# Performance work log

Hardware: AMD Instinct MI355X
Metric: run time of the kernel (lower is better)

Reference implementation:

```python
import jax, jax.numpy as jnp
import numpy as np

DIM = 2048
N_HEADS = 16
N_KV_HEADS = 8
HEAD_DIM = DIM // N_HEADS  # 128
N_REP = N_HEADS // N_KV_HEADS
THETA = 10000.0


def _rope_cos_sin(seq_len, head_dim):
    # freqs_cis = polar(1, outer(t, 1/theta^(2i/d))), i in [0, head_dim//2)
    inv = 1.0 / (THETA ** (jnp.arange(0, head_dim, 2, dtype=jnp.float32) / head_dim))
    t = jnp.arange(seq_len, dtype=jnp.float32)
    freqs = jnp.outer(t, inv)  # [S, hd/2]
    return jnp.cos(freqs), jnp.sin(freqs)


def _apply_rope(x, cos, sin):
    # x: [B, S, H, hd]; pairs (even, odd) treated as complex and multiplied by e^{i*freq}
    xr = x[..., 0::2]
    xi = x[..., 1::2]
    c = cos[None, :, None, :]
    s = sin[None, :, None, :]
    out_r = xr * c - xi * s
    out_i = xr * s + xi * c
    return jnp.stack([out_r, out_i], axis=-1).reshape(x.shape)


def setup_inputs() -> dict:
    key = jax.random.key(0)
    ks = jax.random.split(key, 5)
    B, S = 2, 2048
    sc = 0.02
    return {
        "x": jax.random.normal(ks[0], (B, S, DIM), dtype=jnp.float32),
        "wq": jax.random.normal(ks[1], (N_HEADS * HEAD_DIM, DIM), dtype=jnp.float32) * sc,
        "wk": jax.random.normal(ks[2], (N_KV_HEADS * HEAD_DIM, DIM), dtype=jnp.float32) * sc,
        "wv": jax.random.normal(ks[3], (N_KV_HEADS * HEAD_DIM, DIM), dtype=jnp.float32) * sc,
        "wo": jax.random.normal(ks[4], (DIM, N_HEADS * HEAD_DIM), dtype=jnp.float32) * sc,
        "start_pos": 0,
        "inference": 0,
    }


def reference(x, wq, wk, wv, wo, start_pos, inference):
    B, S, _ = x.shape
    xq = (x @ wq.T).reshape(B, S, N_HEADS, HEAD_DIM)
    xk = (x @ wk.T).reshape(B, S, N_KV_HEADS, HEAD_DIM)
    xv = (x @ wv.T).reshape(B, S, N_KV_HEADS, HEAD_DIM)

    cos, sin = _rope_cos_sin(S, HEAD_DIM)
    xq = _apply_rope(xq, cos, sin)
    xk = _apply_rope(xk, cos, sin)

    # repeat_kv (GQA): [B,S,Hkv,hd] -> [B,S,Hkv*n_rep,hd]
    xk = jnp.repeat(xk, N_REP, axis=2)
    xv = jnp.repeat(xv, N_REP, axis=2)

    q = xq.transpose(0, 2, 1, 3)  # [B,H,S,hd]
    k = xk.transpose(0, 2, 1, 3)
    v = xv.transpose(0, 2, 1, 3)

    scores = jnp.einsum("bhqd,bhkd->bhqk", q, k) / np.sqrt(HEAD_DIM).astype(np.float32)
    mask = jnp.triu(jnp.full((S, S), -jnp.inf, dtype=scores.dtype), k=1)
    scores = scores + mask
    probs = jax.nn.softmax(scores.astype(jnp.float32), axis=-1).astype(q.dtype)

    out = jnp.einsum("bhqk,bhkd->bhqd", probs, v)
    out = out.transpose(0, 2, 1, 3).reshape(B, S, N_HEADS * HEAD_DIM)
    return out @ wo.T
```

## Files before the change

### kernel.cpp

```cpp
#include <hip/hip_runtime.h>
#include <hip/hip_bf16.h>
#include <stdint.h>
#include <type_traits>

typedef __attribute__((ext_vector_type(4))) float   f32x4;
typedef __attribute__((ext_vector_type(8))) __bf16  bf16x8;
typedef __attribute__((ext_vector_type(4))) unsigned int u32x4;

#define B_   2
#define S_   2048
#define DIM_ 2048
#define NH_  16
#define NKV_ 8
#define HD_  128

__device__ inline unsigned short f2bf(float f) {
    unsigned u = __float_as_uint(f);
    unsigned r = (u + 0x7fffu + ((u >> 16) & 1u)) >> 16;
    return (unsigned short)r;
}
__device__ inline float bf2f(unsigned short s) {
    return __uint_as_float(((unsigned)s) << 16);
}

__global__ void k_convert(const float* __restrict__ x,  const float* __restrict__ wq,
                          const float* __restrict__ wk, const float* __restrict__ wv,
                          const float* __restrict__ wo,
                          unsigned short* __restrict__ xb,  unsigned short* __restrict__ wqkb,
                          unsigned short* __restrict__ wvb, unsigned short* __restrict__ wob)
{
    int i = blockIdx.x * blockDim.x + threadIdx.x;
    const int NX = 2097152, NWQ = 1048576, NWK = 524288, NWV = 524288, NWO = 1048576;
    const float* src; unsigned short* dst; int j = i;
    if (j < NX) { src = x; dst = xb; }
    else {
        j -= NX;
        if (j < NWQ) { src = wq; dst = wqkb; }
        else {
            j -= NWQ;
            if (j < NWK) { src = wk; dst = wqkb + (size_t)2048 * 2048; }
            else {
                j -= NWK;
                if (j < NWV) { src = wv; dst = wvb; }
                else { j -= NWV; if (j >= NWO) return; src = wo; dst = wob; }
            }
        }
    }
    float4 v = reinterpret_cast<const float4*>(src)[j];
    ushort4 o;
    o.x = f2bf(v.x); o.y = f2bf(v.y); o.z = f2bf(v.z); o.w = f2bf(v.w);
    reinterpret_cast<ushort4*>(dst)[j] = o;
}

__global__ void k_rope_table(float* __restrict__ tab)
{
    int t = blockIdx.x * blockDim.x + threadIdx.x;
    if (t >= S_ * 64) return;
    int i = t & 63;
    int s = t >> 6;
    float inv = expf(-((float)i / 64.0f) * 9.210340371976184f);
    float ang = (float)s * inv;
    tab[2 * t]     = cosf(ang);
    tab[2 * t + 1] = sinf(ang);
}

#define BAR  __builtin_amdgcn_s_barrier()
#define WLG  asm volatile("s_waitcnt lgkmcnt(0)" ::: "memory")
#define WVM4 asm volatile("s_waitcnt vmcnt(4)" ::: "memory")
#define WVM0 asm volatile("s_waitcnt vmcnt(0)" ::: "memory")

#define G_LDS(SRC, DST) __builtin_amdgcn_global_load_lds( \
    (const __attribute__((address_space(1))) void*)(SRC), \
    (__attribute__((address_space(3))) void*)(DST), 16, 0, 0)

#define STAGE(MATB, DBUF, HALF, KT) do { \
    const unsigned short* _s0 = ((MATB) ? pb0 : pa0) + (size_t)(HALF) * 128 * 2048 + (KT) * 64; \
    const unsigned short* _s1 = ((MATB) ? pb1 : pa1) + (size_t)(HALF) * 128 * 2048 + (KT) * 64; \
    G_LDS(_s0, lds + (MATB) * 32768 + (DBUF) * 16384 + (HALF) * 8192 + lo0); \
    G_LDS(_s1, lds + (MATB) * 32768 + (DBUF) * 16384 + (HALF) * 8192 + lo1); \
} while (0)

#define LDA(DBUF, MH) { \
    _Pragma("unroll") \
    for (int mf = 0; mf < 4; ++mf) { \
        _Pragma("unroll") \
        for (int kk = 0; kk < 2; ++kk) { \
            const int R = wm * 128 + (MH) * 64 + mf * 16 + lr; \
            afr[MH][mf][kk] = *reinterpret_cast<const bf16x8*>( \
                &lds[(DBUF) * 16384 + R * 64 + (((kk * 4 + g) ^ (lr & 7)) * 8)]); \
        } } }

#define LDB(DBUF, NH) { \
    _Pragma("unroll") \
    for (int nf = 0; nf < 2; ++nf) { \
        _Pragma("unroll") \
        for (int kk = 0; kk < 2; ++kk) { \
            const int R = wn * 64 + (NH) * 32 + nf * 16 + lr; \
            bfr[NH][nf][kk] = *reinterpret_cast<const bf16x8*>( \
                &lds[32768 + (DBUF) * 16384 + R * 64 + (((kk * 4 + g) ^ (lr & 7)) * 8)]); \
        } } }

#define MMA(MH, NH) { \
    __builtin_amdgcn_s_setprio(1); \
    _Pragma("unroll") \
    for (int mf = 0; mf < 4; ++mf) { \
        _Pragma("unroll") \
        for (int nf = 0; nf < 2; ++nf) { \
            _Pragma("unroll") \
            for (int kk = 0; kk < 2; ++kk) \
                acc[(MH) * 4 + mf][(NH) * 2 + nf] = __builtin_amdgcn_mfma_f32_16x16x32_bf16( \
                    afr[MH][mf][kk], bfr[NH][nf][kk], acc[(MH) * 4 + mf][(NH) * 2 + nf], 0, 0, 0); \
        } } \
    __builtin_amdgcn_s_setprio(0); }

template <int MODE>
__global__ __launch_bounds__(512, 2) void k_gemm256(
    const unsigned short* __restrict__ A0g, const unsigned short* __restrict__ B0g,
    const unsigned short* __restrict__ A1g, const unsigned short* __restrict__ B1g,
    unsigned short* __restrict__ Cq, unsigned short* __restrict__ Cv,
    float* __restrict__ Cf, const float* __restrict__ tab)
{
    __shared__ __attribute__((aligned(16))) unsigned short lds[65536];

    const int tid  = threadIdx.x;
    const int lane = tid & 63;
    const int wid  = tid >> 6;
    const int g    = lane >> 4;
    const int lr   = lane & 15;
    const int wm   = wid >> 2;
    const int wn   = wid & 3;

    const unsigned short *Ag, *Bg;
    int brow, bcol;
    bool isQK = true;
    if constexpr (MODE == 0) {
        int swz = (blockIdx.x & 7) * 32 + (blockIdx.x >> 3);
        if (swz < 192) { Ag = A0g; Bg = B0g; brow = (swz / 12) << 8; bcol = (swz % 12) << 8; }
        else { int ix = swz - 192; isQK = false; Ag = A1g; Bg = B1g; brow = (ix >> 4) << 8; bcol = (ix & 15) << 8; }
    } else {
        int swz = (blockIdx.x & 7) * 16 + (blockIdx.x >> 3);
        Ag = A0g; Bg = B0g; brow = (swz >> 3) << 8; bcol = (swz & 7) << 8;
    }

    const int E0 = wid * 512 + lane * 8;
    const int E1 = E0 + 4096;
    const int r0 = E0 >> 6, r1 = E1 >> 6;
    const int c0 = ((((E0 >> 3) & 7) ^ (r0 & 7)) * 8);
    const int c1 = ((((E1 >> 3) & 7) ^ (r1 & 7)) * 8);
    const unsigned short* pa0 = Ag + (size_t)(brow + r0) * 2048 + c0;
    const unsigned short* pa1 = Ag + (size_t)(brow + r1) * 2048 + c1;
    const unsigned short* pb0 = Bg + (size_t)(bcol + r0) * 2048 + c0;
    const unsigned short* pb1 = Bg + (size_t)(bcol + r1) * 2048 + c1;
    const int lo0 = wid * 512;
    const int lo1 = lo0 + 4096;

    f32x4 acc[8][4] = {};
    bf16x8 afr[2][4][2];
    bf16x8 bfr[2][2][2];

    STAGE(0, 0, 0, 0); STAGE(0, 0, 1, 0); STAGE(1, 0, 0, 0); STAGE(1, 0, 1, 0);
    STAGE(0, 1, 0, 1); STAGE(1, 1, 0, 1);
    WVM0; BAR;

    #pragma unroll 1
    for (int i = 0; i < 16; ++i) {
        const int kt1 = 2 * i + 1;
        int kt2 = 2 * i + 2;  if (kt2 >= 32) kt2 -= 32;
        int kt3 = 2 * i + 3;  if (kt3 >= 32) kt3 -= 32;
        LDA(0, 0); LDB(0, 0);
        STAGE(0, 1, 1, kt1);
        BAR; WLG; MMA(0, 0); BAR;
        LDA(0, 1);
        STAGE(1, 1, 1, kt1);
        BAR; WLG; MMA(1, 0); BAR;
        LDB(0, 1);
        STAGE(1, 0, 0, kt2);
        BAR; WLG; MMA(0, 1); BAR;
        STAGE(0, 0, 0, kt2);
        WVM4;
        BAR; WLG; MMA(1, 1); BAR;
        LDA(1, 0); LDB(1, 0);
        STAGE(0, 0, 1, kt2);
        BAR; WLG; MMA(0, 0); BAR;
        LDA(1, 1);
        STAGE(1, 0, 1, kt2);
        BAR; WLG; MMA(1, 0); BAR;
        LDB(1, 1);
        STAGE(1, 1, 0, kt3);
        BAR; WLG; MMA(0, 1); BAR;
        STAGE(0, 1, 0, kt3);
        WVM4;
        BAR; WLG; MMA(1, 1); BAR;
    }

    if constexpr (MODE == 1) {
        #pragma unroll
        for (int m = 0; m < 8; ++m)
            #pragma unroll
            for (int n = 0; n < 4; ++n)
                #pragma unroll
                for (int r = 0; r < 4; ++r) {
                    int row = brow + wm * 128 + (m >> 2) * 64 + (m & 3) * 16 + g * 4 + r;
                    int col = bcol + wn * 64 + (n >> 1) * 32 + (n & 1) * 16 + lr;
                    Cf[(size_t)row * 2048 + col] = acc[m][n][r];
                }
    } else if (isQK) {
        #pragma unroll
        for (int m = 0; m < 8; ++m) {
            #pragma unroll
            for (int n = 0; n < 4; ++n) {
                int col = bcol + wn * 64 + (n >> 1) * 32 + (n & 1) * 16 + lr;
                int ci  = (col & 127) >> 1;
                int row0 = brow + wm * 128 + (m >> 2) * 64 + (m & 3) * 16 + g * 4;
                #pragma unroll
                for (int r = 0; r < 4; ++r) {
                    int row = row0 + r;
                    int s   = row & (S_ - 1);
                    float2 cs = *reinterpret_cast<const float2*>(&tab[(s * 64 + ci) * 2]);
                    float v = acc[m][n][r];
                    float o = __shfl_xor(v, 1);
                    float res = (lane & 1) ? fmaf(o, cs.y, v * cs.x)
                                           : fmaf(v, cs.x, -(o * cs.y));
                    Cq[(size_t)row * 3072 + col] = f2bf(res);
                }
            }
        }
    } else {
        #pragma unroll
        for (int m = 0; m < 8; ++m)
            #pragma unroll
            for (int n = 0; n < 4; ++n)
                #pragma unroll
                for (int r = 0; r < 4; ++r) {
                    int row = brow + wm * 128 + (m >> 2) * 64 + (m & 3) * 16 + g * 4 + r;
                    int col = bcol + wn * 64 + (n >> 1) * 32 + (n & 1) * 16 + lr;
                    Cv[(size_t)row * 4096 + col] = f2bf(acc[m][n][r]);
                }
    }
}

__global__ __launch_bounds__(512, 4) void k_attn(
    const unsigned short* __restrict__ QK,
    const unsigned short* __restrict__ Vt,
    unsigned short* __restrict__ O)
{
    __shared__ __attribute__((aligned(16))) unsigned short Ks[64 * 128];
    __shared__ __attribute__((aligned(16))) unsigned short Vs[128 * 64];

    const int tid  = threadIdx.x;
    const int lane = tid & 63;
    const int wid  = tid >> 6;
    const int g    = lane >> 4;
    const int lr   = lane & 15;

    const int bid    = blockIdx.x;
    const int qt_raw = bid & 15;
    const int h      = (bid >> 4) & 15;
    const int b      = bid >> 8;
    const int qt     = b ? (15 - qt_raw) : qt_raw;
    const int hk     = h >> 1;
    const int q0w    = qt * 128 + wid * 16;

    bf16x8 qf[4];
    #pragma unroll
    for (int c = 0; c < 4; ++c)
        qf[c] = *reinterpret_cast<const bf16x8*>(
            QK + (size_t)(b * S_ + q0w + lr) * 3072 + h * HD_ + c * 32 + g * 8);

    f32x4 o_acc[8] = {};
    float m_run = -INFINITY;
    float l_run = 0.f;

    const float C2 = 1.4426950408889634f * 0.08838834764831845f;
    const int nt = 2 * qt + 2;
    const int srcb = (g & 1) * 32 + lr;
    const bool hig = g >> 1;

    #pragma unroll 1
    for (int t = 0; t < nt; ++t) {
        const int kv0 = t * 64;
        __syncthreads();
        #pragma unroll
        for (int i4 = 0; i4 < 2; ++i4) {
            const int base = (i4 * 8 + wid) * 512;
            const int E = base + lane * 8;
            {
                int row = E >> 7, ch = (E >> 3) & 15;
                int col = ((ch ^ (row & 15)) * 8);
                G_LDS(QK + (size_t)(b * S_ + kv0 + row) * 3072 + 2048 + hk * HD_ + col,
                      &Ks[base]);
            }
            {
                int d = E >> 6, ch = (E >> 3) & 7;
                int kv = ((ch ^ (d & 7)) * 8);
                G_LDS(Vt + (size_t)(hk * HD_ + d) * (B_ * S_) + b * S_ + kv0 + kv,
                      &Vs[base]);
            }
        }
        __syncthreads();

        const bool active = kv0 < q0w + 16;
        if (active) {
            f32x4 sv[4] = {};
            __builtin_amdgcn_s_setprio(1);
            #pragma unroll
            for (int c = 0; c < 4; ++c)
                #pragma unroll
                for (int kvb = 0; kvb < 4; ++kvb) {
                    bf16x8 kf = *reinterpret_cast<const bf16x8*>(
                        &Ks[(kvb * 16 + lr) * 128 + (((c * 4 + g) ^ lr) * 8)]);
                    sv[kvb] = __builtin_amdgcn_mfma_f32_16x16x32_bf16(
                        kf, qf[c], sv[kvb], 0, 0, 0);
                }
            __builtin_amdgcn_s_setprio(0);

            if (kv0 + 63 > q0w) {
                int qg = q0w + lr;
                #pragma unroll
                for (int kvb = 0; kvb < 4; ++kvb) {
                    int kvg0 = kv0 + kvb * 16 + g * 4;
                    #pragma unroll
                    for (int r = 0; r < 4; ++r)
                        if (kvg0 + r > qg) sv[kvb][r] = -INFINITY;
                }
            }

            float m0 = fmaxf(fmaxf(fmaxf(sv[0][0], sv[0][1]), fmaxf(sv[0][2], sv[0][3])),
                             fmaxf(fmaxf(sv[1][0], sv[1][1]), fmaxf(sv[1][2], sv[1][3])));
            m0 = fmaxf(m0, fmaxf(fmaxf(sv[2][0], sv[2][1]), fmaxf(sv[2][2], sv[2][3])));
            m0 = fmaxf(m0, fmaxf(fmaxf(sv[3][0], sv[3][1]), fmaxf(sv[3][2], sv[3][3])));
            m0 = fmaxf(m0, __shfl_xor(m0, 16));
            m0 = fmaxf(m0, __shfl_xor(m0, 32));

            if (__any(m0 > m_run + 90.5f)) {
                float mn = fmaxf(m_run, m0);
                float al = exp2f((m_run - mn) * C2);
                m_run = mn;
                l_run *= al;
                #pragma unroll
                for (int db = 0; db < 8; ++db)
                    #pragma unroll
                    for (int r = 0; r < 4; ++r)
                        o_acc[db][r] *= al;
            }

            unsigned pk[4][2];
            float mb2 = m_run * C2;
            float rs = 0.f;
            #pragma unroll
            for (int kvb = 0; kvb < 4; ++kvb) {
                float p0 = exp2f(fmaf(sv[kvb][0], C2, -mb2));
                float p1 = exp2f(fmaf(sv[kvb][1], C2, -mb2));
                float p2 = exp2f(fmaf(sv[kvb][2], C2, -mb2));
                float p3 = exp2f(fmaf(sv[kvb][3], C2, -mb2));
                rs += (p0 + p1) + (p2 + p3);
                pk[kvb][0] = (unsigned)f2bf(p0) | ((unsigned)f2bf(p1) << 16);
                pk[kvb][1] = (unsigned)f2bf(p2) | ((unsigned)f2bf(p3) << 16);
            }
            rs += __shfl_xor(rs, 16);
            rs += __shfl_xor(rs, 32);
            l_run += rs;

            #pragma unroll
            for (int kk = 0; kk < 2; ++kk) {
                u32x4 w;
                unsigned a0 = (unsigned)__shfl((int)pk[2 * kk][0], srcb);
                unsigned a1 = (unsigned)__shfl((int)pk[2 * kk][1], srcb);
                unsigned a2 = (unsigned)__shfl((int)pk[2 * kk][0], srcb + 16);
                unsigned a3 = (unsigned)__shfl((int)pk[2 * kk][1], srcb + 16);
                unsigned b0 = (unsigned)__shfl((int)pk[2 * kk + 1][0], srcb);
                unsigned b1 = (unsigned)__shfl((int)pk[2 * kk + 1][1], srcb);
                unsigned b2 = (unsigned)__shfl((int)pk[2 * kk + 1][0], srcb + 16);
                unsigned b3 = (unsigned)__shfl((int)pk[2 * kk + 1][1], srcb + 16);
                w[0] = hig ? b0 : a0;
                w[1] = hig ? b1 : a1;
                w[2] = hig ? b2 : a2;
                w[3] = hig ? b3 : a3;
                bf16x8 pb = *reinterpret_cast<const bf16x8*>(&w);
                __builtin_amdgcn_s_setprio(1);
                #pragma unroll
                for (int db = 0; db < 8; ++db) {
                    bf16x8 vf = *reinterpret_cast<const bf16x8*>(
                        &Vs[(db * 16 + lr) * 64 + (((kk * 4 + g) ^ (lr & 7)) * 8)]);
                    o_acc[db] = __builtin_amdgcn_mfma_f32_16x16x32_bf16(
                        vf, pb, o_acc[db], 0, 0, 0);
                }
                __builtin_amdgcn_s_setprio(0);
            }
        }
    }

    {
        float inv = 1.f / l_run;
        size_t rowb = ((size_t)(b * S_ + q0w + lr) * NH_ + h) * HD_;
        #pragma unroll
        for (int db = 0; db < 8; ++db) {
            ushort4 o4;
            o4.x = f2bf(o_acc[db][0] * inv);
            o4.y = f2bf(o_acc[db][1] * inv);
            o4.z = f2bf(o_acc[db][2] * inv);
            o4.w = f2bf(o_acc[db][3] * inv);
            *reinterpret_cast<ushort4*>(&O[rowb + db * 16 + g * 4]) = o4;
        }
    }
}

extern "C" void kernel_launch(void* const* d_in, const int* in_sizes, int n_in,
                              void* d_out, int out_size, void* d_ws, size_t ws_size,
                              hipStream_t stream)
{
    const float* x  = (const float*)d_in[0];
    const float* wq = (const float*)d_in[1];
    const float* wk = (const float*)d_in[2];
    const float* wv = (const float*)d_in[3];
    const float* wo = (const float*)d_in[4];
    float* out = (float*)d_out;

    char* ws = (char*)d_ws;
    size_t off = 0;
    auto alloc = [&](size_t bytes) -> void* {
        void* p = ws + off;
        off += (bytes + 255) & ~(size_t)255;
        return p;
    };
    unsigned short* xb   = (unsigned short*)alloc((size_t)B_ * S_ * DIM_ * 2);
    unsigned short* wqkb = (unsigned short*)alloc((size_t)3072 * 2048 * 2);
    unsigned short* wvb  = (unsigned short*)alloc((size_t)1024 * 2048 * 2);
    unsigned short* wob  = (unsigned short*)alloc((size_t)DIM_ * DIM_ * 2);
    unsigned short* QKb  = (unsigned short*)alloc((size_t)B_ * S_ * 3072 * 2);
    unsigned short* Vtb  = (unsigned short*)alloc((size_t)1024 * B_ * S_ * 2);
    unsigned short* Ob   = (unsigned short*)alloc((size_t)B_ * S_ * NH_ * HD_ * 2);
    float* tab = (float*)alloc((size_t)S_ * 64 * 2 * 4);

    k_convert<<<20480, 256, 0, stream>>>(x, wq, wk, wv, wo, xb, wqkb, wvb, wob);
    k_rope_table<<<(S_ * 64 + 255) / 256, 256, 0, stream>>>(tab);
    k_gemm256<0><<<256, 512, 0, stream>>>(xb, wqkb, wvb, xb, QKb, Vtb, nullptr, tab);
    k_attn<<<B_ * NH_ * (S_ / 128), 512, 0, stream>>>(QKb, Vtb, Ob);
    k_gemm256<1><<<128, 512, 0, stream>>>(Ob, wob, nullptr, nullptr, nullptr, nullptr, out, tab);

    (void)in_sizes; (void)n_in; (void)out_size; (void)ws_size;
}
```

Baseline: 227.8 us.

## Fuse rope table into convert kernel and retile output projection GEMM

The rope cos/sin table computation is folded into the conversion kernel, which removes one launch. The output projection moves from the shared 256x256-tile template to a dedicated kernel with 128x256 tiles and 256 blocks, so the grid better fills the 256 CUs of the GPU. The new kernel uses smaller per-wave accumulators and its own LDS double-buffer schedule with vmcnt(6) waits, trading data reuse per tile for more parallelism.

```diff
diff --git a/kernel.cpp b/kernel.cpp
--- a/kernel.cpp
+++ b/kernel.cpp
@@ -27,10 +27,23 @@
                           const float* __restrict__ wk, const float* __restrict__ wv,
                           const float* __restrict__ wo,
                           unsigned short* __restrict__ xb,  unsigned short* __restrict__ wqkb,
-                          unsigned short* __restrict__ wvb, unsigned short* __restrict__ wob)
+                          unsigned short* __restrict__ wvb, unsigned short* __restrict__ wob,
+                          float* __restrict__ tab)
 {
     int i = blockIdx.x * blockDim.x + threadIdx.x;
     const int NX = 2097152, NWQ = 1048576, NWK = 524288, NWV = 524288, NWO = 1048576;
+    const int NTOT = NX + NWQ + NWK + NWV + NWO;
+    if (i >= NTOT) {
+        int t = i - NTOT;
+        if (t >= S_ * 64) return;
+        int ii = t & 63;
+        int s = t >> 6;
+        float inv = expf(-((float)ii / 64.0f) * 9.210340371976184f);
+        float ang = (float)s * inv;
+        tab[2 * t]     = cosf(ang);
+        tab[2 * t + 1] = sinf(ang);
+        return;
+    }
     const float* src; unsigned short* dst; int j = i;
     if (j < NX) { src = x; dst = xb; }
     else {
@@ -42,7 +55,7 @@
             else {
                 j -= NWK;
                 if (j < NWV) { src = wv; dst = wvb; }
-                else { j -= NWV; if (j >= NWO) return; src = wo; dst = wob; }
+                else { j -= NWV; src = wo; dst = wob; }
             }
         }
     }
@@ -52,21 +65,10 @@
     reinterpret_cast<ushort4*>(dst)[j] = o;
 }
 
-__global__ void k_rope_table(float* __restrict__ tab)
-{
-    int t = blockIdx.x * blockDim.x + threadIdx.x;
-    if (t >= S_ * 64) return;
-    int i = t & 63;
-    int s = t >> 6;
-    float inv = expf(-((float)i / 64.0f) * 9.210340371976184f);
-    float ang = (float)s * inv;
-    tab[2 * t]     = cosf(ang);
-    tab[2 * t + 1] = sinf(ang);
-}
-
 #define BAR  __builtin_amdgcn_s_barrier()
 #define WLG  asm volatile("s_waitcnt lgkmcnt(0)" ::: "memory")
 #define WVM4 asm volatile("s_waitcnt vmcnt(4)" ::: "memory")
+#define WVM6 asm volatile("s_waitcnt vmcnt(6)" ::: "memory")
 #define WVM0 asm volatile("s_waitcnt vmcnt(0)" ::: "memory")
 
 #define G_LDS(SRC, DST) __builtin_amdgcn_global_load_lds( \
@@ -113,12 +115,11 @@
         } } \
     __builtin_amdgcn_s_setprio(0); }
 
-template <int MODE>
-__global__ __launch_bounds__(512, 2) void k_gemm256(
+__global__ __launch_bounds__(512, 2) void k_gemm_qkv(
     const unsigned short* __restrict__ A0g, const unsigned short* __restrict__ B0g,
-    const unsigned short* __restrict__ A1g, const unsigned short* __restrict__ B1g,
+    const unsigned short* __restrict__ A1g,
     unsigned short* __restrict__ Cq, unsigned short* __restrict__ Cv,
-    float* __restrict__ Cf, const float* __restrict__ tab)
+    const float* __restrict__ tab)
 {
     __shared__ __attribute__((aligned(16))) unsigned short lds[65536];
 
@@ -133,13 +134,10 @@
     const unsigned short *Ag, *Bg;
     int brow, bcol;
     bool isQK = true;
-    if constexpr (MODE == 0) {
+    {
         int swz = (blockIdx.x & 7) * 32 + (blockIdx.x >> 3);
         if (swz < 192) { Ag = A0g; Bg = B0g; brow = (swz / 12) << 8; bcol = (swz % 12) << 8; }
-        else { int ix = swz - 192; isQK = false; Ag = A1g; Bg = B1g; brow = (ix >> 4) << 8; bcol = (ix & 15) << 8; }
-    } else {
-        int swz = (blockIdx.x & 7) * 16 + (blockIdx.x >> 3);
-        Ag = A0g; Bg = B0g; brow = (swz >> 3) << 8; bcol = (swz & 7) << 8;
+        else { int ix = swz - 192; isQK = false; Ag = A1g; Bg = A0g; brow = (ix >> 4) << 8; bcol = (ix & 15) << 8; }
     }
 
     const int E0 = wid * 512 + lane * 8;
@@ -193,18 +191,7 @@
         BAR; WLG; MMA(1, 1); BAR;
     }
 
-    if constexpr (MODE == 1) {
-        #pragma unroll
-        for (int m = 0; m < 8; ++m)
-            #pragma unroll
-            for (int n = 0; n < 4; ++n)
-                #pragma unroll
-                for (int r = 0; r < 4; ++r) {
-                    int row = brow + wm * 128 + (m >> 2) * 64 + (m & 3) * 16 + g * 4 + r;
-                    int col = bcol + wn * 64 + (n >> 1) * 32 + (n & 1) * 16 + lr;
-                    Cf[(size_t)row * 2048 + col] = acc[m][n][r];
-                }
-    } else if (isQK) {
+    if (isQK) {
         #pragma unroll
         for (int m = 0; m < 8; ++m) {
             #pragma unroll
@@ -237,6 +224,128 @@
                     Cv[(size_t)row * 4096 + col] = f2bf(acc[m][n][r]);
                 }
     }
+}
+
+#define OP_LDA(D, MH) { \
+    _Pragma("unroll") \
+    for (int mf = 0; mf < 2; ++mf) { \
+        _Pragma("unroll") \
+        for (int kk = 0; kk < 2; ++kk) { \
+            const int R = wm * 64 + (MH) * 32 + mf * 16 + lr; \
+            afr[mf][kk] = *reinterpret_cast<const bf16x8*>( \
+                &lds[(D) * 8192 + R * 64 + (((kk * 4 + g) ^ (lr & 7)) * 8)]); \
+        } } }
+
+#define OP_LDB(D, NH, BFR) { \
+    _Pragma("unroll") \
+    for (int nf = 0; nf < 2; ++nf) { \
+        _Pragma("unroll") \
+        for (int kk = 0; kk < 2; ++kk) { \
+            const int R = wn * 64 + (NH) * 32 + nf * 16 + lr; \
+            BFR[nf][kk] = *reinterpret_cast<const bf16x8*>( \
+                &lds[16384 + (D) * 16384 + R * 64 + (((kk * 4 + g) ^ (lr & 7)) * 8)]); \
+        } } }
+
+#define OP_MMA(MH, NH, BFR) { \
+    __builtin_amdgcn_s_setprio(1); \
+    _Pragma("unroll") \
+    for (int mf = 0; mf < 2; ++mf) { \
+        _Pragma("unroll") \
+        for (int nf = 0; nf < 2; ++nf) { \
+            _Pragma("unroll") \
+            for (int kk = 0; kk < 2; ++kk) \
+                acc[(MH) * 2 + mf][(NH) * 2 + nf] = __builtin_amdgcn_mfma_f32_16x16x32_bf16( \
+                    afr[mf][kk], BFR[nf][kk], acc[(MH) * 2 + mf][(NH) * 2 + nf], 0, 0, 0); \
+        } } \
+    __builtin_amdgcn_s_setprio(0); }
+
+#define OP_SA(D, KT) do { \
+    G_LDS(pa0 + (KT) * 64, lds + (D) * 8192 + t8); \
+    G_LDS(pa1 + (KT) * 64, lds + (D) * 8192 + 4096 + t8); \
+} while (0)
+#define OP_SB01(D, KT) do { \
+    G_LDS(pb0 + (KT) * 64, lds + 16384 + (D) * 16384 + t8); \
+    G_LDS(pb1 + (KT) * 64, lds + 16384 + (D) * 16384 + 4096 + t8); \
+} while (0)
+#define OP_SB23(D, KT) do { \
+    G_LDS(pb2 + (KT) * 64, lds + 16384 + (D) * 16384 + 8192 + t8); \
+    G_LDS(pb3 + (KT) * 64, lds + 16384 + (D) * 16384 + 12288 + t8); \
+} while (0)
+
+__global__ __launch_bounds__(512, 1) void k_gemm_op(
+    const unsigned short* __restrict__ Ag,
+    const unsigned short* __restrict__ Bg,
+    float* __restrict__ C)
+{
+    __shared__ __attribute__((aligned(16))) unsigned short lds[49152];
+
+    const int tid  = threadIdx.x;
+    const int lane = tid & 63;
+    const int wid  = tid >> 6;
+    const int g    = lane >> 4;
+    const int lr   = lane & 15;
+    const int wm   = wid >> 2;
+    const int wn   = wid & 3;
+
+    const int swz  = (blockIdx.x & 7) * 32 + (blockIdx.x >> 3);
+    const int brow = (swz >> 3) << 7;
+    const int bcol = (swz & 7) << 8;
+
+    const int E = tid * 8;
+    const int r = E >> 6;
+    const int c = (((E >> 3) & 7) ^ (r & 7)) * 8;
+    const int t8 = tid * 8;
+    const unsigned short* pa0 = Ag + (size_t)(brow + r)       * 2048 + c;
+    const unsigned short* pa1 = Ag + (size_t)(brow + 64 + r)  * 2048 + c;
+    const unsigned short* pb0 = Bg + (size_t)(bcol + r)       * 2048 + c;
+    const unsigned short* pb1 = Bg + (size_t)(bcol + 64 + r)  * 2048 + c;
+    const unsigned short* pb2 = Bg + (size_t)(bcol + 128 + r) * 2048 + c;
+    const unsigned short* pb3 = Bg + (size_t)(bcol + 192 + r) * 2048 + c;
+
+    f32x4 acc[4][4] = {};
+    bf16x8 afr[2][2];
+    bf16x8 bfr0[2][2], bfr1[2][2];
+
+    OP_SA(0, 0); OP_SB01(0, 0); OP_SB23(0, 0);
+    OP_SA(1, 1); OP_SB01(1, 1); OP_SB23(1, 1);
+    WVM0; BAR;
+
+    #pragma unroll 1
+    for (int i = 0; i < 16; ++i) {
+        int kt2 = 2 * i + 2;  if (kt2 >= 32) kt2 -= 32;
+        int kt3 = 2 * i + 3;  if (kt3 >= 32) kt3 -= 32;
+        OP_LDA(0, 0); OP_LDB(0, 0, bfr0);
+        BAR; WLG; OP_MMA(0, 0, bfr0); BAR;
+        OP_LDB(0, 1, bfr1);
+        BAR; WLG; OP_MMA(0, 1, bfr1); BAR;
+        OP_LDA(0, 1);
+        OP_SB01(0, kt2);
+        BAR; WLG; OP_MMA(1, 0, bfr0); BAR;
+        OP_SB23(0, kt2); OP_SA(0, kt2);
+        WVM6;
+        BAR; WLG; OP_MMA(1, 1, bfr1); BAR;
+        OP_LDA(1, 0); OP_LDB(1, 0, bfr0);
+        BAR; WLG; OP_MMA(0, 0, bfr0); BAR;
+        OP_LDB(1, 1, bfr1);
+        BAR; WLG; OP_MMA(0, 1, bfr1); BAR;
+        OP_LDA(1, 1);
+        OP_SB01(1, kt3);
+        BAR; WLG; OP_MMA(1, 0, bfr0); BAR;
+        OP_SB23(1, kt3); OP_SA(1, kt3);
+        WVM6;
+        BAR; WLG; OP_MMA(1, 1, bfr1); BAR;
+    }
+
+    #pragma unroll
+    for (int m = 0; m < 4; ++m)
+        #pragma unroll
+        for (int n = 0; n < 4; ++n)
+            #pragma unroll
+            for (int rr = 0; rr < 4; ++rr) {
+                int row = brow + wm * 64 + m * 16 + g * 4 + rr;
+                int col = bcol + wn * 64 + n * 16 + lr;
+                C[(size_t)row * 2048 + col] = acc[m][n][rr];
+            }
 }
 
 __global__ __launch_bounds__(512, 4) void k_attn(
@@ -432,11 +541,10 @@
     unsigned short* Ob   = (unsigned short*)alloc((size_t)B_ * S_ * NH_ * HD_ * 2);
     float* tab = (float*)alloc((size_t)S_ * 64 * 2 * 4);
 
-    k_convert<<<20480, 256, 0, stream>>>(x, wq, wk, wv, wo, xb, wqkb, wvb, wob);
-    k_rope_table<<<(S_ * 64 + 255) / 256, 256, 0, stream>>>(tab);
-    k_gemm256<0><<<256, 512, 0, stream>>>(xb, wqkb, wvb, xb, QKb, Vtb, nullptr, tab);
+    k_convert<<<20992, 256, 0, stream>>>(x, wq, wk, wv, wo, xb, wqkb, wvb, wob, tab);
+    k_gemm_qkv<<<256, 512, 0, stream>>>(xb, wqkb, wvb, QKb, Vtb, tab);
     k_attn<<<B_ * NH_ * (S_ / 128), 512, 0, stream>>>(QKb, Vtb, Ob);
-    k_gemm256<1><<<128, 512, 0, stream>>>(Ob, wob, nullptr, nullptr, nullptr, nullptr, out, tab);
+    k_gemm_op<<<256, 512, 0, stream>>>(Ob, wob, out);
 
     (void)in_sizes; (void)n_in; (void)out_size; (void)ws_size;
 }
```

New measurement: 209.3 us. 8.1% less time.
